# Optimization experiments

Measured on AMD Instinct MI355X. Metric: run time of the kernel, lower is better.

Reference implementation:

```python
import jax, jax.numpy as jnp
import numpy as np

FRAME_LENGTH = 512
HOP_LENGTH = 256
ENERGY_THRESHOLD = 0.01
SAMPLE_RATE = 16000
SILENCE_FRAMES = int(0.3 * SAMPLE_RATE / HOP_LENGTH)      # 18
MIN_SPEECH_FRAMES = int(0.1 * SAMPLE_RATE / HOP_LENGTH)   # 6


def setup_inputs() -> dict:
    key = jax.random.key(0)
    waveform = jax.random.normal(key, (32, 960000), dtype=jnp.float32)
    return {"waveform": waveform}


def _compute_energy(waveform):
    # (B, S) -> (B, T): short-time mean-square energy, full frames only
    n = waveform.shape[-1]
    num_frames = max(1, (n - FRAME_LENGTH) // HOP_LENGTH + 1)
    idx = jnp.arange(num_frames)[:, None] * HOP_LENGTH + jnp.arange(FRAME_LENGTH)[None, :]
    frames = waveform[:, idx]                     # (B, T, F)
    return jnp.mean(frames * frames, axis=-1)


def _threshold(e):
    # torch.quantile(non_zero, 0.2) with linear interpolation; fallback to fixed threshold
    n = e.shape[0]
    s = jnp.sort(e)
    nzero = jnp.sum(s <= 0)          # number of entries excluded by (> 0)
    nz = n - nzero                   # count of positive entries
    pos = 0.2 * (nz - 1).astype(jnp.float32)
    lo = jnp.floor(pos).astype(jnp.int32)
    hi = jnp.ceil(pos).astype(jnp.int32)
    frac = pos - lo.astype(jnp.float32)
    ilo = jnp.clip(nzero + lo, 0, n - 1)
    ihi = jnp.clip(nzero + hi, 0, n - 1)
    q = s[ilo] * (1.0 - frac) + s[ihi] * frac
    return jnp.where(nz > 0, q, jnp.float32(ENERGY_THRESHOLD))


def _vad_one(e):
    # Faithful scan-based version of the per-frame hysteresis state machine.
    n = e.shape[0]
    m = e > _threshold(e)

    def step(state, xs):
        in_sp, start, sil = state
        t, mt = xs
        start2 = jnp.where(mt & ~in_sp, t, start)
        sil2 = jnp.where(mt, jnp.int32(0), jnp.where(in_sp, sil + 1, sil))
        closed = (~mt) & in_sp & (sil2 >= SILENCE_FRAMES)
        end = t - sil2  # matches original: end = t - silence_count (exclusive)
        in_sp2 = jnp.where(mt, True, jnp.where(closed, False, in_sp))
        return (in_sp2, start2, sil2), (closed, start2, end)

    init = (jnp.bool_(False), jnp.int32(0), jnp.int32(0))
    (in_sp_f, start_f, _), (closed, starts, ends) = jax.lax.scan(
        step, init, (jnp.arange(n, dtype=jnp.int32), m))

    # trailing open segment -> (start, n)
    starts = jnp.concatenate([starts, start_f[None]])
    ends = jnp.concatenate([ends, jnp.full((1,), n, dtype=jnp.int32)])
    valid = jnp.concatenate([closed, in_sp_f[None]])
    valid = valid & ((ends - starts) >= MIN_SPEECH_FRAMES)

    # mark mask[start:end] = True via +1/-1 diff then cumsum (RLE)
    sentinel = n + 1
    idx_s = jnp.where(valid, jnp.clip(starts, 0, n), sentinel)
    idx_e = jnp.where(valid, jnp.clip(ends, 0, n), sentinel)
    d = jnp.zeros(n + 2, dtype=jnp.int32)
    d = d.at[idx_s].add(1).at[idx_e].add(-1)
    return jnp.cumsum(d)[:n] > 0


def reference(waveform):
    energy = _compute_energy(waveform)     # (B, T)
    return jax.vmap(_vad_one)(energy)      # (B, T) bool VAD mask
```

## Files before the change

kernel.cpp:

```cpp
#include <hip/hip_runtime.h>

#define NFRAMES 3749
#define NBLOCKS 3750
#define NSAMP   960000
#define NBATCH  32
#define NWORDS  59
#define SILENCE_FRAMES 18
#define MIN_SPEECH_FRAMES 6
#define MAXSEG  256

__global__ __launch_bounds__(256) void vad_block_sums(const float* __restrict__ wav,
                                                      double* __restrict__ bs) {
    int tid = threadIdx.x;
    int w = tid >> 6, lane = tid & 63;
    const float4* q = (const float4*)(wav + (size_t)blockIdx.x * 4096);
    #pragma unroll
    for (int i = 0; i < 4; ++i) {
        float4 v = q[(i << 8) + tid];
        double a = (double)(v.x * v.x) + (double)(v.y * v.y)
                 + (double)(v.z * v.z) + (double)(v.w * v.w);
        #pragma unroll
        for (int m = 1; m < 64; m <<= 1)
            a += __shfl_xor(a, m, 64);
        if (lane == 0)
            bs[(size_t)blockIdx.x * 16 + (i << 2) + w] = a;
    }
}

__global__ __launch_bounds__(512) void vad_finish(const double* __restrict__ bs,
                                                  int* __restrict__ out) {
    __shared__ __attribute__((aligned(16))) int hist[4][8][256];
    __shared__ unsigned long long mw[NWORDS];
    __shared__ unsigned long long sw[NWORDS];
    __shared__ unsigned long long lw[NWORDS];
    __shared__ unsigned long long Sw[NWORDS];
    __shared__ unsigned long long Ew[NWORDS];
    __shared__ int wbS[NWORDS], wbL[NWORDS];
    __shared__ int startpos[MAXSEG], lastpos[MAXSEG];
    __shared__ int nzero_sh, nseg_sh;
    __shared__ unsigned sel_prefix_sh;
    __shared__ int sel_k_sh;
    __shared__ int cLE_sh;
    __shared__ unsigned minGT_sh;
    __shared__ float thr_sh;

    int b = blockIdx.x;
    int tid = threadIdx.x;
    int lane = tid & 63, wv = tid >> 6;
    const double* row = bs + (size_t)b * NBLOCKS;

    if (tid == 0) { nzero_sh = 0; sel_prefix_sh = 0u; cLE_sh = 0; minGT_sh = 0xFFFFFFFFu; }
    #pragma unroll
    for (int i = 0; i < 4; ++i)
        ((int4*)hist)[(i << 9) + tid] = make_int4(0, 0, 0, 0);

    unsigned ub[8];
    int myzero = 0;
    #pragma unroll
    for (int i = 0; i < 8; ++i) {
        int t = tid + (i << 9);
        unsigned u = 0xFFFFFFFFu;
        if (t < NFRAMES) {
            double s = row[t] + row[t + 1];
            float e = (float)(s * (1.0 / 512.0));
            u = __float_as_uint(e);
            if (e <= 0.0f) myzero++;
        }
        ub[i] = u;
    }
    #pragma unroll
    for (int m = 1; m < 64; m <<= 1)
        myzero += __shfl_xor(myzero, m, 64);
    if (lane == 0 && myzero) atomicAdd(&nzero_sh, myzero);
    __syncthreads();

    int nzero = nzero_sh;
    int nz = NFRAMES - nzero;

    if (nz > 0) {
        float pos = 0.2f * (float)(nz - 1);
        int lo = (int)floorf(pos), hi = (int)ceilf(pos);
        int rank_lo = min(max(nzero + lo, 0), NFRAMES - 1);
        int rank_hi = min(max(nzero + hi, 0), NFRAMES - 1);
        if (tid == 0) sel_k_sh = rank_lo;

        int pno = 0;
        for (int shift = 24; shift >= 0; shift -= 8, ++pno) {
            unsigned pref = sel_prefix_sh;
            unsigned pmask = (shift == 24) ? 0u : (0xFFFFFFFFu << (shift + 8));
            int* hw = hist[pno][wv];
            #pragma unroll
            for (int j = 0; j < 8; ++j) {
                unsigned u = ub[j];
                bool act = ((int)u >= 0) && ((u & pmask) == (pref & pmask));
                unsigned long long ball = __ballot(act);
                if (ball != 0ull) {
                    unsigned bin = (u >> shift) & 255u;
                    int leader = (int)__ffsll(ball) - 1;
                    unsigned fbin = (unsigned)__shfl((int)bin, leader, 64);
                    unsigned long long same = __ballot(act && (bin == fbin));
                    if (same == ball) {
                        if (lane == leader) atomicAdd(&hw[fbin], (int)__popcll(ball));
                    } else if (act) {
                        atomicAdd(&hw[bin], 1);
                    }
                }
            }
            __syncthreads();
            if (wv == 0) {
                int bin0 = lane << 2;
                int h0 = 0, h1 = 0, h2 = 0, h3 = 0;
                #pragma unroll
                for (int c = 0; c < 8; ++c) {
                    int4 hc = *(const int4*)&hist[pno][c][bin0];
                    h0 += hc.x; h1 += hc.y; h2 += hc.z; h3 += hc.w;
                }
                int tot = h0 + h1 + h2 + h3;
                int inc = tot;
                #pragma unroll
                for (int off = 1; off < 64; off <<= 1) {
                    int y = __shfl_up(inc, off, 64);
                    if (lane >= off) inc += y;
                }
                int run = inc - tot;
                int k = sel_k_sh;
                int hh[4] = {h0, h1, h2, h3};
                #pragma unroll
                for (int j2 = 0; j2 < 4; ++j2) {
                    if (k >= run && k < run + hh[j2]) {
                        sel_prefix_sh = pref | ((unsigned)(bin0 + j2) << shift);
                        sel_k_sh = k - run;
                    }
                    run += hh[j2];
                }
            }
            __syncthreads();
        }

        unsigned vb = sel_prefix_sh;

        if (rank_hi != rank_lo) {
            int c = 0;
            unsigned mg = 0xFFFFFFFFu;
            #pragma unroll
            for (int j = 0; j < 8; ++j) {
                unsigned u = ub[j];
                if ((int)u >= 0) {
                    if (u <= vb) c++;
                    else mg = min(mg, u);
                }
            }
            #pragma unroll
            for (int off = 32; off > 0; off >>= 1) {
                c += __shfl_xor(c, off, 64);
                mg = min(mg, (unsigned)__shfl_xor((int)mg, off, 64));
            }
            if (lane == 0) {
                atomicAdd(&cLE_sh, c);
                atomicMin(&minGT_sh, mg);
            }
            __syncthreads();
        }

        if (tid == 0) {
            float vlo = __uint_as_float(vb);
            float vhi;
            if (rank_hi == rank_lo) vhi = vlo;
            else vhi = (cLE_sh >= rank_lo + 2) ? vlo : __uint_as_float(minGT_sh);
            float frac = pos - (float)lo;
            thr_sh = vlo * (1.0f - frac) + vhi * frac;
        }
    } else {
        if (tid == 0) thr_sh = 0.01f;
    }
    __syncthreads();
    float thr = thr_sh;

    #pragma unroll
    for (int i = 0; i < 8; ++i) {
        unsigned u = ub[i];
        bool p = ((int)u >= 0) && (__uint_as_float(u) > thr);
        unsigned long long bm = __ballot(p);
        int wi = wv + (i << 3);
        if (lane == 0 && wi < NWORDS) mw[wi] = bm;
    }
    __syncthreads();

    for (int wi = wv; wi < NWORDS; wi += 8) {
        unsigned long long W  = mw[wi];
        unsigned long long Wm = (wi > 0) ? mw[wi - 1] : 0ull;
        unsigned long long Wp = (wi + 1 < NWORDS) ? mw[wi + 1] : 0ull;
        int l = lane;
        bool mt = (W >> l) & 1ull;
        bool prev_any, next_any;
        if (l >= 18) {
            prev_any = ((W >> (l - 18)) & 0x3FFFFull) != 0ull;
        } else {
            unsigned long long lowpart = W & ((1ull << l) - 1ull);
            unsigned long long hipart  = Wm >> (46 + l);
            prev_any = (lowpart | hipart) != 0ull;
        }
        if (l <= 45) {
            next_any = ((W >> (l + 1)) & 0x3FFFFull) != 0ull;
        } else {
            unsigned long long a  = (l < 63) ? (W >> (l + 1)) : 0ull;
            unsigned long long bb = Wp & ((1ull << (l - 45)) - 1ull);
            next_any = (a | bb) != 0ull;
        }
        unsigned long long bS = __ballot(mt && !prev_any);
        unsigned long long bL = __ballot(mt && !next_any);
        if (lane == 0) { sw[wi] = bS; lw[wi] = bL; }
    }
    __syncthreads();

    if (wv < 2) {
        const unsigned long long* src = (wv == 0) ? sw : lw;
        unsigned long long w_ = (lane < NWORDS) ? src[lane] : 0ull;
        int c = __popcll(w_);
        int inc = c;
        #pragma unroll
        for (int off = 1; off < 64; off <<= 1) {
            int y = __shfl_up(inc, off, 64);
            if (lane >= off) inc += y;
        }
        int* dst = (wv == 0) ? wbS : wbL;
        if (lane < NWORDS) dst[lane] = inc - c;
        if (wv == 0 && lane == NWORDS - 1) nseg_sh = inc;
    }
    __syncthreads();

    for (int wi = wv; wi < NWORDS; wi += 8) {
        unsigned long long wS = sw[wi], wL = lw[wi];
        int t = (wi << 6) + lane;
        unsigned long long lmask = (1ull << lane) - 1ull;
        if ((wS >> lane) & 1ull) startpos[wbS[wi] + __popcll(wS & lmask)] = t;
        if ((wL >> lane) & 1ull) lastpos[wbL[wi] + __popcll(wL & lmask)] = t;
    }
    for (int wi = tid; wi < NWORDS; wi += 512) { Sw[wi] = 0ull; Ew[wi] = 0ull; }
    __syncthreads();

    int nseg = nseg_sh;
    for (int k = tid; k < nseg; k += 512) {
        int s = startpos[k], L = lastpos[k];
        int e = (L >= NFRAMES - SILENCE_FRAMES) ? NFRAMES : L;
        if (e - s >= MIN_SPEECH_FRAMES) {
            atomicOr(&Sw[s >> 6], 1ull << (s & 63));
            atomicOr(&Ew[e >> 6], 1ull << (e & 63));
        }
    }
    __syncthreads();

    if (wv < 2) {
        const unsigned long long* src = (wv == 0) ? Sw : Ew;
        unsigned long long w_ = (lane < NWORDS) ? src[lane] : 0ull;
        int c = __popcll(w_);
        int inc = c;
        #pragma unroll
        for (int off = 1; off < 64; off <<= 1) {
            int y = __shfl_up(inc, off, 64);
            if (lane >= off) inc += y;
        }
        int* dst = (wv == 0) ? wbS : wbL;
        if (lane < NWORDS) dst[lane] = inc - c;
    }
    __syncthreads();

    int* orow = out + (size_t)b * NFRAMES;
    for (int wi = wv; wi < NWORDS; wi += 8) {
        unsigned long long wS2 = Sw[wi], wE2 = Ew[wi];
        int t = (wi << 6) + lane;
        unsigned long long ile = (lane == 63) ? ~0ull : ((1ull << (lane + 1)) - 1ull);
        int cS = wbS[wi] + __popcll(wS2 & ile);
        int cE = wbL[wi] + __popcll(wE2 & ile);
        if (t < NFRAMES) orow[t] = (cS > cE) ? 1 : 0;
    }
}

extern "C" void kernel_launch(void* const* d_in, const int* in_sizes, int n_in,
                              void* d_out, int out_size, void* d_ws, size_t ws_size,
                              hipStream_t stream) {
    const float* wav = (const float*)d_in[0];
    int* out = (int*)d_out;
    double* bs = (double*)d_ws;

    vad_block_sums<<<(NBATCH * NSAMP) / 4096, 256, 0, stream>>>(wav, bs);
    vad_finish<<<NBATCH, 512, 0, stream>>>(bs, out);
}
```

Measured before the change: 185.2 us.

## Cut barriers in VAD finish kernel via wave-redundant radix select and single-wave segmenting

The first radix-select histogram pass now runs during the energy load loop. Every wave redundantly scans the histogram and broadcasts the selected prefix with ballot/shuffle, which removes the shared-memory handoff and one barrier per pass. Per-wave histograms are shared by pairs of waves, so the zeroing work is halved. Segment start/end detection, compaction and the prefix scans now run in one wave using shuffles, which drops several block-wide barriers and shared arrays. The cost is redundant work across waves, more atomic contention per histogram copy, and serial bit loops in one wave.

```diff
diff --git a/kernel.cpp b/kernel.cpp
--- a/kernel.cpp
+++ b/kernel.cpp
@@ -29,33 +29,32 @@
 
 __global__ __launch_bounds__(512) void vad_finish(const double* __restrict__ bs,
                                                   int* __restrict__ out) {
-    __shared__ __attribute__((aligned(16))) int hist[4][8][256];
+    __shared__ __attribute__((aligned(16))) int hist[4][4][256];
     __shared__ unsigned long long mw[NWORDS];
-    __shared__ unsigned long long sw[NWORDS];
-    __shared__ unsigned long long lw[NWORDS];
     __shared__ unsigned long long Sw[NWORDS];
     __shared__ unsigned long long Ew[NWORDS];
     __shared__ int wbS[NWORDS], wbL[NWORDS];
     __shared__ int startpos[MAXSEG], lastpos[MAXSEG];
-    __shared__ int nzero_sh, nseg_sh;
-    __shared__ unsigned sel_prefix_sh;
-    __shared__ int sel_k_sh;
+    __shared__ int nzero_sh;
     __shared__ int cLE_sh;
     __shared__ unsigned minGT_sh;
-    __shared__ float thr_sh;
 
     int b = blockIdx.x;
     int tid = threadIdx.x;
     int lane = tid & 63, wv = tid >> 6;
     const double* row = bs + (size_t)b * NBLOCKS;
 
-    if (tid == 0) { nzero_sh = 0; sel_prefix_sh = 0u; cLE_sh = 0; minGT_sh = 0xFFFFFFFFu; }
-    #pragma unroll
-    for (int i = 0; i < 4; ++i)
-        ((int4*)hist)[(i << 9) + tid] = make_int4(0, 0, 0, 0);
+    {
+        int4* hz = (int4*)hist;
+        hz[tid] = make_int4(0, 0, 0, 0);
+        hz[tid + 512] = make_int4(0, 0, 0, 0);
+    }
+    if (tid == 0) { nzero_sh = 0; cLE_sh = 0; minGT_sh = 0xFFFFFFFFu; }
+    __syncthreads();
 
     unsigned ub[8];
     int myzero = 0;
+    int* h0w = hist[0][wv >> 1];
     #pragma unroll
     for (int i = 0; i < 8; ++i) {
         int t = tid + (i << 9);
@@ -67,6 +66,19 @@
             if (e <= 0.0f) myzero++;
         }
         ub[i] = u;
+        bool act = ((int)u >= 0);
+        unsigned long long ball = __ballot(act);
+        if (ball != 0ull) {
+            unsigned bin = u >> 24;
+            int leader = (int)__ffsll(ball) - 1;
+            unsigned fbin = (unsigned)__shfl((int)bin, leader, 64);
+            unsigned long long same = __ballot(act && (bin == fbin));
+            if (same == ball) {
+                if (lane == leader) atomicAdd(&h0w[fbin], (int)__popcll(ball));
+            } else if (act) {
+                atomicAdd(&h0w[bin], 1);
+            }
+        }
     }
     #pragma unroll
     for (int m = 1; m < 64; m <<= 1)
@@ -76,68 +88,74 @@
 
     int nzero = nzero_sh;
     int nz = NFRAMES - nzero;
+    float thr;
 
     if (nz > 0) {
         float pos = 0.2f * (float)(nz - 1);
         int lo = (int)floorf(pos), hi = (int)ceilf(pos);
         int rank_lo = min(max(nzero + lo, 0), NFRAMES - 1);
         int rank_hi = min(max(nzero + hi, 0), NFRAMES - 1);
-        if (tid == 0) sel_k_sh = rank_lo;
-
-        int pno = 0;
-        for (int shift = 24; shift >= 0; shift -= 8, ++pno) {
-            unsigned pref = sel_prefix_sh;
-            unsigned pmask = (shift == 24) ? 0u : (0xFFFFFFFFu << (shift + 8));
-            int* hw = hist[pno][wv];
-            #pragma unroll
-            for (int j = 0; j < 8; ++j) {
-                unsigned u = ub[j];
-                bool act = ((int)u >= 0) && ((u & pmask) == (pref & pmask));
-                unsigned long long ball = __ballot(act);
-                if (ball != 0ull) {
-                    unsigned bin = (u >> shift) & 255u;
-                    int leader = (int)__ffsll(ball) - 1;
-                    unsigned fbin = (unsigned)__shfl((int)bin, leader, 64);
-                    unsigned long long same = __ballot(act && (bin == fbin));
-                    if (same == ball) {
-                        if (lane == leader) atomicAdd(&hw[fbin], (int)__popcll(ball));
-                    } else if (act) {
-                        atomicAdd(&hw[bin], 1);
+
+        unsigned pref = 0u;
+        int k = rank_lo;
+
+        #pragma unroll
+        for (int p = 0; p < 4; ++p) {
+            int shift = 24 - (p << 3);
+            if (p > 0) {
+                unsigned pmask = 0xFFFFFFFFu << (shift + 8);
+                int* hw = hist[p][wv >> 1];
+                #pragma unroll
+                for (int j = 0; j < 8; ++j) {
+                    unsigned u = ub[j];
+                    bool act = ((int)u >= 0) && ((u & pmask) == (pref & pmask));
+                    unsigned long long ball = __ballot(act);
+                    if (ball != 0ull) {
+                        unsigned bin = (u >> shift) & 255u;
+                        int leader = (int)__ffsll(ball) - 1;
+                        unsigned fbin = (unsigned)__shfl((int)bin, leader, 64);
+                        unsigned long long same = __ballot(act && (bin == fbin));
+                        if (same == ball) {
+                            if (lane == leader) atomicAdd(&hw[fbin], (int)__popcll(ball));
+                        } else if (act) {
+                            atomicAdd(&hw[bin], 1);
+                        }
                     }
                 }
-            }
-            __syncthreads();
-            if (wv == 0) {
-                int bin0 = lane << 2;
-                int h0 = 0, h1 = 0, h2 = 0, h3 = 0;
-                #pragma unroll
-                for (int c = 0; c < 8; ++c) {
-                    int4 hc = *(const int4*)&hist[pno][c][bin0];
-                    h0 += hc.x; h1 += hc.y; h2 += hc.z; h3 += hc.w;
+                __syncthreads();
+            }
+            int bin0 = lane << 2;
+            int4 a0 = *(const int4*)&hist[p][0][bin0];
+            int4 a1 = *(const int4*)&hist[p][1][bin0];
+            int4 a2 = *(const int4*)&hist[p][2][bin0];
+            int4 a3 = *(const int4*)&hist[p][3][bin0];
+            int h[4] = { a0.x + a1.x + a2.x + a3.x, a0.y + a1.y + a2.y + a3.y,
+                         a0.z + a1.z + a2.z + a3.z, a0.w + a1.w + a2.w + a3.w };
+            int tot = h[0] + h[1] + h[2] + h[3];
+            int inc = tot;
+            #pragma unroll
+            for (int off = 1; off < 64; off <<= 1) {
+                int y = __shfl_up(inc, off, 64);
+                if (lane >= off) inc += y;
+            }
+            int run = inc - tot;
+            unsigned my_pref = 0u; int my_k = 0; bool found = false;
+            #pragma unroll
+            for (int j2 = 0; j2 < 4; ++j2) {
+                if (!found && k >= run && k < run + h[j2]) {
+                    my_pref = pref | ((unsigned)(bin0 + j2) << shift);
+                    my_k = k - run;
+                    found = true;
                 }
-                int tot = h0 + h1 + h2 + h3;
-                int inc = tot;
-                #pragma unroll
-                for (int off = 1; off < 64; off <<= 1) {
-                    int y = __shfl_up(inc, off, 64);
-                    if (lane >= off) inc += y;
-                }
-                int run = inc - tot;
-                int k = sel_k_sh;
-                int hh[4] = {h0, h1, h2, h3};
-                #pragma unroll
-                for (int j2 = 0; j2 < 4; ++j2) {
-                    if (k >= run && k < run + hh[j2]) {
-                        sel_prefix_sh = pref | ((unsigned)(bin0 + j2) << shift);
-                        sel_k_sh = k - run;
-                    }
-                    run += hh[j2];
-                }
-            }
-            __syncthreads();
-        }
-
-        unsigned vb = sel_prefix_sh;
+                run += h[j2];
+            }
+            unsigned long long fb = __ballot(found);
+            int leader = (int)__ffsll(fb) - 1;
+            pref = (unsigned)__shfl((int)my_pref, leader, 64);
+            k = __shfl(my_k, leader, 64);
+        }
+
+        unsigned vb = pref;
 
         if (rank_hi != rank_lo) {
             int c = 0;
@@ -160,108 +178,84 @@
                 atomicMin(&minGT_sh, mg);
             }
             __syncthreads();
-        }
-
-        if (tid == 0) {
             float vlo = __uint_as_float(vb);
-            float vhi;
-            if (rank_hi == rank_lo) vhi = vlo;
-            else vhi = (cLE_sh >= rank_lo + 2) ? vlo : __uint_as_float(minGT_sh);
+            float vhi = (cLE_sh >= rank_lo + 2) ? vlo : __uint_as_float(minGT_sh);
             float frac = pos - (float)lo;
-            thr_sh = vlo * (1.0f - frac) + vhi * frac;
+            thr = vlo * (1.0f - frac) + vhi * frac;
+        } else {
+            float vlo = __uint_as_float(vb);
+            float frac = pos - (float)lo;
+            thr = vlo * (1.0f - frac) + vlo * frac;
         }
     } else {
-        if (tid == 0) thr_sh = 0.01f;
-    }
-    __syncthreads();
-    float thr = thr_sh;
+        thr = 0.01f;
+    }
 
     #pragma unroll
     for (int i = 0; i < 8; ++i) {
         unsigned u = ub[i];
-        bool p = ((int)u >= 0) && (__uint_as_float(u) > thr);
-        unsigned long long bm = __ballot(p);
+        bool pm = ((int)u >= 0) && (__uint_as_float(u) > thr);
+        unsigned long long bm = __ballot(pm);
         int wi = wv + (i << 3);
         if (lane == 0 && wi < NWORDS) mw[wi] = bm;
     }
-    __syncthreads();
-
-    for (int wi = wv; wi < NWORDS; wi += 8) {
-        unsigned long long W  = mw[wi];
-        unsigned long long Wm = (wi > 0) ? mw[wi - 1] : 0ull;
-        unsigned long long Wp = (wi + 1 < NWORDS) ? mw[wi + 1] : 0ull;
+    if (tid < NWORDS) { Sw[tid] = 0ull; Ew[tid] = 0ull; }
+    __syncthreads();
+
+    if (wv == 0) {
         int l = lane;
-        bool mt = (W >> l) & 1ull;
-        bool prev_any, next_any;
-        if (l >= 18) {
-            prev_any = ((W >> (l - 18)) & 0x3FFFFull) != 0ull;
-        } else {
-            unsigned long long lowpart = W & ((1ull << l) - 1ull);
-            unsigned long long hipart  = Wm >> (46 + l);
-            prev_any = (lowpart | hipart) != 0ull;
-        }
-        if (l <= 45) {
-            next_any = ((W >> (l + 1)) & 0x3FFFFull) != 0ull;
-        } else {
-            unsigned long long a  = (l < 63) ? (W >> (l + 1)) : 0ull;
-            unsigned long long bb = Wp & ((1ull << (l - 45)) - 1ull);
-            next_any = (a | bb) != 0ull;
-        }
-        unsigned long long bS = __ballot(mt && !prev_any);
-        unsigned long long bL = __ballot(mt && !next_any);
-        if (lane == 0) { sw[wi] = bS; lw[wi] = bL; }
-    }
-    __syncthreads();
-
-    if (wv < 2) {
-        const unsigned long long* src = (wv == 0) ? sw : lw;
-        unsigned long long w_ = (lane < NWORDS) ? src[lane] : 0ull;
-        int c = __popcll(w_);
-        int inc = c;
+        unsigned long long W  = (l < NWORDS) ? mw[l] : 0ull;
+        unsigned long long Wm = __shfl_up(W, 1, 64);   if (l == 0) Wm = 0ull;
+        unsigned long long Wp = __shfl_down(W, 1, 64);
+
+        unsigned long long pa = 0ull, na = 0ull;
+        #pragma unroll
+        for (int d = 1; d <= SILENCE_FRAMES; ++d) {
+            pa |= (W << d) | (Wm >> (64 - d));
+            na |= (W >> d) | (Wp << (64 - d));
+        }
+        unsigned long long sWr = W & ~pa;
+        unsigned long long lWr = W & ~na;
+
+        int cS = __popcll(sWr), cL = __popcll(lWr);
+        int packc = cS | (cL << 16);
+        int incp = packc;
         #pragma unroll
         for (int off = 1; off < 64; off <<= 1) {
-            int y = __shfl_up(inc, off, 64);
-            if (lane >= off) inc += y;
-        }
-        int* dst = (wv == 0) ? wbS : wbL;
-        if (lane < NWORDS) dst[lane] = inc - c;
-        if (wv == 0 && lane == NWORDS - 1) nseg_sh = inc;
-    }
-    __syncthreads();
-
-    for (int wi = wv; wi < NWORDS; wi += 8) {
-        unsigned long long wS = sw[wi], wL = lw[wi];
-        int t = (wi << 6) + lane;
-        unsigned long long lmask = (1ull << lane) - 1ull;
-        if ((wS >> lane) & 1ull) startpos[wbS[wi] + __popcll(wS & lmask)] = t;
-        if ((wL >> lane) & 1ull) lastpos[wbL[wi] + __popcll(wL & lmask)] = t;
-    }
-    for (int wi = tid; wi < NWORDS; wi += 512) { Sw[wi] = 0ull; Ew[wi] = 0ull; }
-    __syncthreads();
-
-    int nseg = nseg_sh;
-    for (int k = tid; k < nseg; k += 512) {
-        int s = startpos[k], L = lastpos[k];
-        int e = (L >= NFRAMES - SILENCE_FRAMES) ? NFRAMES : L;
-        if (e - s >= MIN_SPEECH_FRAMES) {
-            atomicOr(&Sw[s >> 6], 1ull << (s & 63));
-            atomicOr(&Ew[e >> 6], 1ull << (e & 63));
-        }
-    }
-    __syncthreads();
-
-    if (wv < 2) {
-        const unsigned long long* src = (wv == 0) ? Sw : Ew;
-        unsigned long long w_ = (lane < NWORDS) ? src[lane] : 0ull;
-        int c = __popcll(w_);
-        int inc = c;
+            int y = __shfl_up(incp, off, 64);
+            if (l >= off) incp += y;
+        }
+        int exS = (incp & 0xFFFF) - cS;
+        int exL = (incp >> 16) - cL;
+        int nseg = __shfl(incp, 63) & 0xFFFF;
+
+        unsigned long long w1 = sWr; int idx = exS;
+        while (w1) { int bit = (int)__ffsll((long long)w1) - 1;
+                     startpos[idx++] = (l << 6) + bit; w1 &= w1 - 1ull; }
+        unsigned long long w2 = lWr; idx = exL;
+        while (w2) { int bit = (int)__ffsll((long long)w2) - 1;
+                     lastpos[idx++] = (l << 6) + bit; w2 &= w2 - 1ull; }
+
+        for (int kk = l; kk < nseg; kk += 64) {
+            int s = startpos[kk], L = lastpos[kk];
+            int e = (L >= NFRAMES - SILENCE_FRAMES) ? NFRAMES : L;
+            if (e - s >= MIN_SPEECH_FRAMES) {
+                atomicOr(&Sw[s >> 6], 1ull << (s & 63));
+                atomicOr(&Ew[e >> 6], 1ull << (e & 63));
+            }
+        }
+
+        unsigned long long S2 = (l < NWORDS) ? Sw[l] : 0ull;
+        unsigned long long E2 = (l < NWORDS) ? Ew[l] : 0ull;
+        int c2 = __popcll(S2) | (__popcll(E2) << 16);
+        int inc2 = c2;
         #pragma unroll
         for (int off = 1; off < 64; off <<= 1) {
-            int y = __shfl_up(inc, off, 64);
-            if (lane >= off) inc += y;
-        }
-        int* dst = (wv == 0) ? wbS : wbL;
-        if (lane < NWORDS) dst[lane] = inc - c;
+            int y = __shfl_up(inc2, off, 64);
+            if (l >= off) inc2 += y;
+        }
+        int ex2 = inc2 - c2;
+        if (l < NWORDS) { wbS[l] = ex2 & 0xFFFF; wbL[l] = ex2 >> 16; }
     }
     __syncthreads();
 
```

Result: no change. 184.0 us (-0.6%).
